# Kernel tuning notes

Measured on AMD Instinct MI355X. Metric: run time of the kernel, lower is better.

Reference implementation:

```python
import math
import jax, jax.numpy as jnp
from jax import lax
import numpy as np

B, DIM, H, W = 8, 256, 64, 64
D_STATE, D_CONV, EXPAND = 16, 4, 2
D_INNER = EXPAND * DIM
DT_RANK = math.ceil(DIM / 16)
POS_LEN = 16
EPS = 1e-5
GN_GROUPS = 32


def setup_inputs() -> dict:
    key = jax.random.key(0)
    ks = iter(jax.random.split(key, 24))
    rn = lambda shape, s=0.02: jax.random.normal(next(ks), shape, jnp.float32) * s
    inp = {}
    inp["x"] = jax.random.normal(next(ks), (B, DIM, H, W), jnp.float32)
    inp["pos_emb"] = rn((1, DIM, POS_LEN), 1.0)
    inp["ln_g"] = jnp.ones((DIM,), jnp.float32)
    inp["ln_b"] = jnp.zeros((DIM,), jnp.float32)
    inp["m_in_w"] = rn((2, 2 * D_INNER, DIM))
    inp["m_conv_w"] = rn((2, D_INNER, D_CONV), 0.1)
    inp["m_conv_b"] = jnp.zeros((2, D_INNER), jnp.float32)
    inp["m_xproj_w"] = rn((2, DT_RANK + 2 * D_STATE, D_INNER))
    inp["m_dt_w"] = rn((2, D_INNER, DT_RANK), 0.1)
    inp["m_dt_b"] = rn((2, D_INNER), 0.1)
    inp["m_A_log"] = jnp.tile(jnp.log(jnp.arange(1, D_STATE + 1, dtype=jnp.float32))[None, None, :], (2, D_INNER, 1))
    inp["m_D"] = jnp.ones((2, D_INNER), jnp.float32)
    inp["m_out_w"] = rn((2, DIM, D_INNER))
    inp["proj_w"] = rn((DIM, 2 * DIM))
    inp["proj_b"] = jnp.zeros((DIM,), jnp.float32)
    inp["up_dw_w"] = rn((DIM, 1, 3, 3), 0.1)
    inp["up_bn1_g"] = jnp.ones((DIM,), jnp.float32)
    inp["up_bn1_b"] = jnp.zeros((DIM,), jnp.float32)
    inp["up_pw_w"] = rn((DIM, DIM), 0.05)
    inp["up_bn2_g"] = jnp.ones((DIM,), jnp.float32)
    inp["up_bn2_b"] = jnp.zeros((DIM,), jnp.float32)
    inp["down_pw_w"] = rn((DIM, DIM), 0.05)
    inp["down_bn_g"] = jnp.ones((DIM,), jnp.float32)
    inp["down_bn_b"] = jnp.zeros((DIM,), jnp.float32)
    inp["gn_g"] = jnp.ones((DIM,), jnp.float32)
    inp["gn_b"] = jnp.zeros((DIM,), jnp.float32)
    return inp


def reference(x, pos_emb, ln_g, ln_b, m_in_w, m_conv_w, m_conv_b, m_xproj_w, m_dt_w, m_dt_b,
              m_A_log, m_D, m_out_w, proj_w, proj_b, up_dw_w, up_bn1_g, up_bn1_b, up_pw_w,
              up_bn2_g, up_bn2_b, down_pw_w, down_bn_g, down_bn_b, gn_g, gn_b):
    Bx, C, Hh, Ww = x.shape

    def ln(t):  # LayerNorm over last dim (shared self.norm)
        m = jnp.mean(t, -1, keepdims=True)
        v = jnp.mean((t - m) ** 2, -1, keepdims=True)
        return (t - m) * lax.rsqrt(v + EPS) * ln_g + ln_b

    def bn(t, g, b):  # BatchNorm2d in eval mode with default running stats (mean 0, var 1)
        return t * (g / jnp.sqrt(1.0 + EPS))[None, :, None, None] + b[None, :, None, None]

    def gn(t):  # GroupNorm(32, C), shared params (self.bn)
        Bn, Cn, Hn, Wn = t.shape
        tg = t.reshape(Bn, GN_GROUPS, Cn // GN_GROUPS, Hn, Wn)
        m = jnp.mean(tg, (2, 3, 4), keepdims=True)
        v = jnp.mean((tg - m) ** 2, (2, 3, 4), keepdims=True)
        tg = (tg - m) * lax.rsqrt(v + EPS)
        return tg.reshape(Bn, Cn, Hn, Wn) * gn_g[None, :, None, None] + gn_b[None, :, None, None]

    def interp_pos(N):  # F.interpolate(pos_embed, size=N, mode='linear', align_corners=False)
        coords = jnp.maximum((jnp.arange(N, dtype=jnp.float32) + 0.5) * (POS_LEN / N) - 0.5, 0.0)
        i0 = jnp.floor(coords).astype(jnp.int32)
        i1 = jnp.minimum(i0 + 1, POS_LEN - 1)
        wgt = coords - i0.astype(jnp.float32)
        return pos_emb[:, :, i0] * (1.0 - wgt) + pos_emb[:, :, i1] * wgt  # (1,C,N)

    def pe_branch(vals, idx, N):  # vals (B,C,N); indices interp at same size = identity
        t = vals + interp_pos(N) + idx.astype(jnp.float32)
        return ln(jnp.swapaxes(t, 1, 2))  # (B,N,C)

    def mamba(u, d):  # standard mamba_ssm selective scan; u (B,L,C)
        xz = jnp.einsum('blc,ic->bli', u, m_in_w[d])
        xh, zg = jnp.split(xz, 2, -1)
        xc = lax.conv_general_dilated(jnp.swapaxes(xh, 1, 2), m_conv_w[d][:, None, :], (1,),
                                      [(D_CONV - 1, 0)], feature_group_count=D_INNER,
                                      dimension_numbers=('NCH', 'OIH', 'NCH'))
        xc = jnp.swapaxes(jax.nn.silu(xc + m_conv_b[d][None, :, None]), 1, 2)  # (B,L,di)
        dbl = jnp.einsum('bld,ed->ble', xc, m_xproj_w[d])
        dt = dbl[..., :DT_RANK]
        Bm = dbl[..., DT_RANK:DT_RANK + D_STATE]
        Cm = dbl[..., DT_RANK + D_STATE:]
        dt = jax.nn.softplus(jnp.einsum('blr,dr->bld', dt, m_dt_w[d]) + m_dt_b[d])  # (B,L,di)
        A = -jnp.exp(m_A_log[d])  # (di,ds)
        dA = jnp.exp(dt[..., None] * A)  # (B,L,di,ds)
        dBx = dt[..., None] * Bm[:, :, None, :] * xc[..., None]

        def step(h, inps):
            dA_t, dBx_t, C_t = inps
            h = dA_t * h + dBx_t
            return h, jnp.einsum('bds,bs->bd', h, C_t)

        h0 = jnp.zeros((u.shape[0], D_INNER, D_STATE), u.dtype)
        _, ys = lax.scan(step, h0, (jnp.swapaxes(dA, 0, 1), jnp.swapaxes(dBx, 0, 1), jnp.swapaxes(Cm, 0, 1)))
        y = jnp.swapaxes(ys, 0, 1) + xc * m_D[d]
        y = y * jax.nn.silu(zg)
        return jnp.einsum('bld,od->blo', y, m_out_w[d])

    # z branch: depthwise ConvTranspose2d(k3,s2,p1,op1) + BN + ReLU + pw conv + BN, then ReLU6
    z = lax.conv_general_dilated(x, jnp.flip(up_dw_w, (2, 3)), (1, 1), [(1, 2), (1, 2)],
                                 lhs_dilation=(2, 2), feature_group_count=C,
                                 dimension_numbers=('NCHW', 'OIHW', 'NCHW'))  # (B,C,2H,2W)
    z = jax.nn.relu(bn(z, up_bn1_g, up_bn1_b))
    z = jnp.einsum('bchw,oc->bohw', z, up_pw_w)
    z = jnp.clip(bn(z, up_bn2_g, up_bn2_b), 0.0, 6.0)

    col_max = pe_branch(jnp.max(x, 2), jnp.argmax(x, 2), Ww)
    col_min = pe_branch(jnp.min(x, 2), jnp.argmin(x, 2), Ww)
    row_max = pe_branch(jnp.max(x, 3), jnp.argmax(x, 3), Hh)
    row_min = pe_branch(jnp.min(x, 3), jnp.argmin(x, 3), Hh)
    result_max = jnp.concatenate([col_max, row_max], 1)  # (B, W+H, C)
    result_min = jnp.concatenate([col_min, row_min], 1)

    fm_max = ln(mamba(result_max, 0))
    fm_min = ln(mamba(result_min, 0))
    bm_max = ln(mamba(jnp.flip(result_max, 1), 1))
    bm_min = ln(mamba(jnp.flip(result_min, 1), 1))

    res_max = jnp.concatenate([fm_max, jnp.flip(bm_max, 1)], -1) @ proj_w.T + proj_b
    res_min = jnp.concatenate([fm_min, jnp.flip(bm_min, 1)], -1) @ proj_w.T + proj_b
    res_max = ln(res_max)[:, :, None, :]  # (B,L,1,C)
    res_min = ln(res_min)[:, None, :, :]  # (B,1,L,C)

    res = jnp.transpose(res_max + res_min, (0, 3, 1, 2))  # (B,C,L,L), L=H+W=2H
    res = jnp.clip(res + 3.0, 0.0, 6.0) / 6.0 * z  # h_sigmoid gate
    res = gn(res)
    res = jnp.einsum('bchw,oc->bohw', res[:, :, ::2, ::2], down_pw_w)  # pw conv stride 2
    res = bn(res, down_bn_g, down_bn_b)
    res = gn(res)
    res = res + x
    res = gn(res)
    return res
```

## Files before the change

kernel.cpp:

```cpp
#include <hip/hip_runtime.h>
#include <hip/hip_bf16.h>
#include <math.h>

typedef __hip_bfloat16 bf16;
typedef __attribute__((ext_vector_type(8))) short short8_t;
typedef __attribute__((ext_vector_type(4))) short short4_t;
typedef __attribute__((ext_vector_type(4))) float f32x4_t;

#define EPSV 1e-5f
#define BNSC 0.99999500003749968f

__device__ __forceinline__ float bf2f(bf16 v){ return __bfloat162float(v); }
__device__ __forceinline__ bf16 f2bf(float v){ return __float2bfloat16(v); }

__device__ __forceinline__ float blk_sum(float v, float* sm){
  int tid = threadIdx.x;
  #pragma unroll
  for(int o=32;o>0;o>>=1) v += __shfl_down(v, o, 64);
  if((tid&63)==0) sm[tid>>6] = v;
  __syncthreads();
  float s = 0.f;
  int nw = blockDim.x>>6;
  for(int i=0;i<nw;i++) s += sm[i];
  __syncthreads();
  return s;
}

__device__ __forceinline__ float softplusf(float x){
  return (x > 20.f) ? x : __logf(1.f + __expf(x));
}
__device__ __forceinline__ float siluf(float x){
  return x / (1.f + __expf(-x));
}

__global__ void prep_weights(const float* __restrict__ in_w, const float* __restrict__ out_w,
                             const float* __restrict__ pw_w, const float* __restrict__ dpw_w,
                             const float* __restrict__ proj_w,
                             bf16* __restrict__ Winb, bf16* __restrict__ Woutb,
                             bf16* __restrict__ Wub, bf16* __restrict__ Wdb,
                             float* __restrict__ PT, float* __restrict__ gacc){
  int idx = blockIdx.x*256 + threadIdx.x;
  if(idx < 6656) gacc[idx] = 0.f;
  if(idx < 524288){ Winb[idx] = f2bf(in_w[idx]); return; }
  if(idx < 786432){ int i=idx-524288; Woutb[i] = f2bf(out_w[i]); return; }
  if(idx < 851968){ int i=idx-786432; Wub[i] = f2bf(pw_w[i]); return; }
  if(idx < 917504){ int i=idx-851968; Wdb[i] = f2bf(dpw_w[i]); return; }
  int k = idx - 917504;
  int i = k >> 9, j = k & 511;
  PT[j*256 + i] = proj_w[k];
}

__global__ __launch_bounds__(256)
void r1_reduce_pe(const float* __restrict__ x, const float* __restrict__ pe,
                  float* __restrict__ pmax, float* __restrict__ pmin,
                  float* __restrict__ xs, float* __restrict__ xq){
  __shared__ float tile[64*65];
  __shared__ float rs_[4], rq_[4];
  int bc = blockIdx.x;
  int b = bc >> 8, c = bc & 255;
  const float* xp = x + ((size_t)bc << 12);
  float s = 0.f, q = 0.f;
  for(int i=threadIdx.x; i<4096; i+=256){
    float v = xp[i];
    tile[(i>>6)*65 + (i&63)] = v;
    s += v; q += v*v;
  }
  #pragma unroll
  for(int o=32;o>0;o>>=1){ s += __shfl_down(s, o, 64); q += __shfl_down(q, o, 64); }
  int wv = threadIdx.x >> 6, t = threadIdx.x & 63;
  if(t == 0){ rs_[wv] = s; rq_[wv] = q; }
  __syncthreads();
  if(threadIdx.x == 0){
    xs[bc] = rs_[0]+rs_[1]+rs_[2]+rs_[3];
    xq[bc] = rq_[0]+rq_[1]+rq_[2]+rq_[3];
  }
  if(wv >= 2) return;
  float coords = fmaxf((t + 0.5f)*0.25f - 0.5f, 0.f);
  int i0 = (int)floorf(coords);
  int i1 = min(i0+1, 15);
  float wg = coords - (float)i0;
  float pos = pe[c*16+i0]*(1.f-wg) + pe[c*16+i1]*wg;
  if(wv == 0){
    float cmx=-3.4e38f, cmn=3.4e38f; int cax=0, can=0;
    for(int h=0;h<64;h++){
      float v = tile[h*65 + t];
      if(v > cmx){ cmx=v; cax=h; }
      if(v < cmn){ cmn=v; can=h; }
    }
    size_t base_col = ((size_t)b*128 + t)*256 + c;
    pmax[base_col] = cmx + pos + (float)cax;
    pmin[base_col] = cmn + pos + (float)can;
  } else {
    float rmx=-3.4e38f, rmn=3.4e38f; int rax=0, ran=0;
    for(int w=0;w<64;w++){
      float v = tile[t*65 + w];
      if(v > rmx){ rmx=v; rax=w; }
      if(v < rmn){ rmn=v; ran=w; }
    }
    size_t base_row = ((size_t)b*128 + 64 + t)*256 + c;
    pmax[base_row] = rmx + pos + (float)rax;
    pmin[base_row] = rmn + pos + (float)ran;
  }
}

__global__ void ln_rows2(float* __restrict__ bufA, float* __restrict__ bufB,
                         const float* __restrict__ g, const float* __restrict__ bb,
                         bf16* __restrict__ boutA, bf16* __restrict__ boutB){
  __shared__ float sm[8];
  int row = blockIdx.x, t = threadIdx.x;
  float* buf; bf16* bout;
  if(row < 1024){ buf = bufA; bout = boutA; }
  else { buf = bufB; bout = boutB; row -= 1024; }
  float v = buf[(size_t)row*256 + t];
  float m = blk_sum(v, sm) * (1.f/256.f);
  float dv = v - m;
  float var = blk_sum(dv*dv, sm) * (1.f/256.f);
  float r = dv * rsqrtf(var + EPSV) * g[t] + bb[t];
  buf[(size_t)row*256 + t] = r;
  if(bout) bout[(size_t)row*256 + t] = f2bf(r);
}

__global__ __launch_bounds__(256,2)
void m1_mfma(const bf16* __restrict__ ubmax, const bf16* __restrict__ ubmin,
             const bf16* __restrict__ Win, float* __restrict__ xz){
  __shared__ bf16 att[64*264];
  int bx = blockIdx.x;
  int it = bx & 3, lt = (bx>>2)&1, b = (bx>>3)&7, r = bx>>6;
  int d = r & 1;
  const bf16* u = (r < 2) ? ubmax : ubmin;
  int flip = r & 1;
  int t = threadIdx.x;
  {
    int pr = t>>5, cc = (t&31)*8;
    #pragma unroll
    for(int i=0;i<8;i++){
      int p = pr + i*8;
      int l = lt*64 + p;
      int le = flip ? (127 - l) : l;
      short8_t v = *(const short8_t*)((const short*)u + ((size_t)(b*128 + le))*256 + cc);
      *(short8_t*)&att[p*264 + cc] = v;
    }
  }
  __syncthreads();
  int wv = t>>6, lane = t&63, quad = lane>>4, l16 = lane&15;
  int m0 = wv*64;
  f32x4_t acc[4][4];
  #pragma unroll
  for(int ms=0;ms<4;ms++)
    #pragma unroll
    for(int ns=0;ns<4;ns++) acc[ms][ns] = (f32x4_t){0.f,0.f,0.f,0.f};
  const short* wbase = (const short*)Win + ((size_t)d*1024 + it*256)*256;
  for(int k0=0;k0<256;k0+=32){
    short8_t afr[4], bfr[4];
    #pragma unroll
    for(int ms=0;ms<4;ms++)
      afr[ms] = *(const short8_t*)(wbase + (size_t)(m0 + ms*16 + l16)*256 + k0 + quad*8);
    #pragma unroll
    for(int ns=0;ns<4;ns++)
      bfr[ns] = *(const short8_t*)&att[(ns*16 + l16)*264 + k0 + quad*8];
    #pragma unroll
    for(int ms=0;ms<4;ms++)
      #pragma unroll
      for(int ns=0;ns<4;ns++)
        acc[ms][ns] = __builtin_amdgcn_mfma_f32_16x16x32_bf16(afr[ms], bfr[ns], acc[ms][ns], 0,0,0);
  }
  int rb = r*8 + b;
  #pragma unroll
  for(int ns=0;ns<4;ns++){
    int l = lt*64 + ns*16 + l16;
    float* dst = xz + ((size_t)rb*128 + l)*1024 + it*256;
    #pragma unroll
    for(int ms=0;ms<4;ms++){
      int i = m0 + ms*16 + quad*4;
      *(f32x4_t*)(dst + i) = acc[ms][ns];
    }
  }
}

#define LSEG4 4
__global__ __launch_bounds__(256)
void m234(const float* __restrict__ xz, const float* __restrict__ cw,
          const float* __restrict__ cb, const float* __restrict__ xproj,
          const float* __restrict__ dtw, const float* __restrict__ dtbias,
          float* __restrict__ xc, float* __restrict__ dbl, float* __restrict__ dt){
  __shared__ float xcs[LSEG4*512];
  __shared__ float pbuf[LSEG4*48*4];
  __shared__ float dblrow[LSEG4*48];
  int bx = blockIdx.x;
  int rb = bx >> 5, seg = bx & 31;
  int l0 = seg * LSEG4;
  int d = (rb >> 3) & 1;
  int t = threadIdx.x;
  #pragma unroll
  for(int j=0; j<(LSEG4*512)/256; j++){
    int i = t + j*256;
    int lr = i >> 9, dd = i & 511;
    int gl = l0 + lr;
    const float* src = xz + ((size_t)rb*128 + gl)*1024 + dd;
    f32x4_t wv = *(const f32x4_t*)(cw + (size_t)(d*512 + dd)*4);
    float s = cb[d*512 + dd];
    float v0 = (gl >= 3) ? src[-3*1024] : 0.f;
    float v1 = (gl >= 2) ? src[-2*1024] : 0.f;
    float v2 = (gl >= 1) ? src[-1*1024] : 0.f;
    float v3 = src[0];
    s += v0*wv[0] + v1*wv[1] + v2*wv[2] + v3*wv[3];
    s = siluf(s);
    xcs[i] = s;
    xc[((size_t)(rb*128 + gl))*512 + dd] = s;
  }
  __syncthreads();
  #pragma unroll
  for(int j=0; j<3; j++){
    int id = t + j*256;
    int row = id / 192;
    int rem = id - row*192;
    int e = rem >> 2, part = rem & 3;
    const float* wp = xproj + ((size_t)(d*48 + e)*512) + part*128;
    const float* xr = xcs + row*512 + part*128;
    float s = 0.f;
    #pragma unroll 4
    for(int k4=0; k4<32; k4++){
      f32x4_t wv = *(const f32x4_t*)(wp + k4*4);
      f32x4_t xv = *(const f32x4_t*)(xr + k4*4);
      s += wv[0]*xv[0] + wv[1]*xv[1] + wv[2]*xv[2] + wv[3]*xv[3];
    }
    pbuf[id] = s;
  }
  __syncthreads();
  for(int i=t; i<LSEG4*48; i+=256){
    int row = i / 48, e = i - row*48;
    int base = row*192 + e*4;
    float s = pbuf[base] + pbuf[base+1] + pbuf[base+2] + pbuf[base+3];
    dblrow[i] = s;
    dbl[((size_t)(rb*128 + l0 + row))*48 + e] = s;
  }
  __syncthreads();
  #pragma unroll
  for(int j=0; j<(LSEG4*512)/256; j++){
    int i = t + j*256;
    int row = i >> 9, dd = i & 511;
    const float* wp = dtw + (size_t)(d*512 + dd)*16;
    const float* dr = dblrow + row*48;
    float s = dtbias[d*512 + dd];
    #pragma unroll
    for(int r4=0; r4<4; r4++){
      f32x4_t wv = *(const f32x4_t*)(wp + r4*4);
      s += dr[r4*4+0]*wv[0] + dr[r4*4+1]*wv[1] + dr[r4*4+2]*wv[2] + dr[r4*4+3]*wv[3];
    }
    dt[((size_t)(rb*128 + l0 + row))*512 + dd] = softplusf(s);
  }
}

__global__ void m5_passA(const float* __restrict__ dt, const float* __restrict__ xc,
                         const float* __restrict__ dbl, const float* __restrict__ Alog,
                         float* __restrict__ P, float* __restrict__ Hl){
  int bx = blockIdx.x;
  int seg = bx & 7, half = (bx>>3)&1, rb = bx>>4;
  int dd = half*256 + threadIdx.x;
  int d = (rb>>3)&1;
  float A[16], h[16], pr[16];
  #pragma unroll
  for(int s=0;s<16;s++){
    A[s] = -__expf(Alog[(size_t)(d*512 + dd)*16 + s]);
    h[s] = 0.f; pr[s] = 1.f;
  }
  int l0 = seg*16;
  for(int l=l0;l<l0+16;l++){
    size_t row = (size_t)rb*128 + l;
    float dtv = dt[row*512 + dd];
    float xcv = xc[row*512 + dd];
    float bx_ = dtv*xcv;
    const float* dr = dbl + row*48;
    #pragma unroll
    for(int s=0;s<16;s++){
      float dA = __expf(dtv*A[s]);
      pr[s] *= dA;
      h[s] = dA*h[s] + bx_*dr[16+s];
    }
  }
  size_t o = ((size_t)(rb*8 + seg)*512 + dd)*16;
  #pragma unroll
  for(int s=0;s<16;s+=4){
    *(f32x4_t*)(P  + o + s) = (f32x4_t){pr[s],pr[s+1],pr[s+2],pr[s+3]};
    *(f32x4_t*)(Hl + o + s) = (f32x4_t){h[s],h[s+1],h[s+2],h[s+3]};
  }
}

__global__ void m5_passB(const float* __restrict__ dt, const float* __restrict__ xc,
                         const float* __restrict__ dbl, const float* __restrict__ xz,
                         const float* __restrict__ Alog, const float* __restrict__ Dp,
                         const float* __restrict__ P, const float* __restrict__ Hl,
                         bf16* __restrict__ ybb){
  int bx = blockIdx.x;
  int seg = bx & 7, half = (bx>>3)&1, rb = bx>>4;
  int dd = half*256 + threadIdx.x;
  int d = (rb>>3)&1;
  float A[16], h[16];
  #pragma unroll
  for(int s=0;s<16;s++){
    A[s] = -__expf(Alog[(size_t)(d*512 + dd)*16 + s]);
    h[s] = 0.f;
  }
  for(int j=0;j<seg;j++){
    size_t o = ((size_t)(rb*8 + j)*512 + dd)*16;
    #pragma unroll
    for(int s=0;s<16;s+=4){
      f32x4_t pv = *(const f32x4_t*)(P + o + s);
      f32x4_t hv = *(const f32x4_t*)(Hl + o + s);
      h[s]   = pv[0]*h[s]   + hv[0];
      h[s+1] = pv[1]*h[s+1] + hv[1];
      h[s+2] = pv[2]*h[s+2] + hv[2];
      h[s+3] = pv[3]*h[s+3] + hv[3];
    }
  }
  float Dv = Dp[d*512 + dd];
  int l0 = seg*16;
  for(int l=l0;l<l0+16;l++){
    size_t row = (size_t)rb*128 + l;
    float dtv = dt[row*512 + dd];
    float xcv = xc[row*512 + dd];
    float zgv = xz[row*1024 + 512 + dd];
    const float* dr = dbl + row*48;
    float bx_ = dtv*xcv;
    float y = 0.f;
    #pragma unroll
    for(int s=0;s<16;s++){
      h[s] = __expf(dtv*A[s])*h[s] + bx_*dr[16+s];
      y += h[s]*dr[32+s];
    }
    ybb[row*512 + dd] = f2bf((y + xcv*Dv) * siluf(zgv));
  }
}

__global__ __launch_bounds__(256,2)
void m6_mfma(const bf16* __restrict__ ybb, const bf16* __restrict__ Wout,
             const float* __restrict__ lng, const float* __restrict__ lnb,
             float* __restrict__ mo){
  __shared__ char smem[64*264*4];
  bf16* ybt = (bf16*)smem;
  float* fbuf = (float*)smem;
  int bx = blockIdx.x;
  int lt = bx & 1, b = (bx>>1)&7, r = bx>>4;
  int d = r & 1, rb = r*8 + b;
  size_t rowbase = (size_t)rb*128 + lt*64;
  int t = threadIdx.x;
  for(int i=t;i<4096;i+=256){
    int row = i>>6, c8 = (i&63)*8;
    short8_t v = *(const short8_t*)((const short*)ybb + (rowbase + row)*512 + c8);
    *(short8_t*)&ybt[row*520 + c8] = v;
  }
  __syncthreads();
  int wv = t>>6, lane = t&63, quad = lane>>4, l16 = lane&15;
  int m0 = wv*64;
  f32x4_t acc[4][4];
  #pragma unroll
  for(int ms=0;ms<4;ms++)
    #pragma unroll
    for(int ns=0;ns<4;ns++) acc[ms][ns] = (f32x4_t){0.f,0.f,0.f,0.f};
  const short* wbase = (const short*)Wout + (size_t)d*256*512;
  for(int k0=0;k0<512;k0+=32){
    short8_t afr[4], bfr[4];
    #pragma unroll
    for(int ms=0;ms<4;ms++)
      afr[ms] = *(const short8_t*)(wbase + (size_t)(m0 + ms*16 + l16)*512 + k0 + quad*8);
    #pragma unroll
    for(int ns=0;ns<4;ns++)
      bfr[ns] = *(const short8_t*)&ybt[(ns*16 + l16)*520 + k0 + quad*8];
    #pragma unroll
    for(int ms=0;ms<4;ms++)
      #pragma unroll
      for(int ns=0;ns<4;ns++)
        acc[ms][ns] = __builtin_amdgcn_mfma_f32_16x16x32_bf16(afr[ms], bfr[ns], acc[ms][ns], 0,0,0);
  }
  __syncthreads();
  #pragma unroll
  for(int ns=0;ns<4;ns++){
    int row = ns*16 + l16;
    #pragma unroll
    for(int ms=0;ms<4;ms++){
      int o = m0 + ms*16 + quad*4;
      *(f32x4_t*)(fbuf + row*264 + o) = acc[ms][ns];
    }
  }
  __syncthreads();
  {
    int row = t >> 2, part = t & 3;
    const float* fr = fbuf + row*264;
    float s = 0.f;
    #pragma unroll 8
    for(int j=0;j<64;j++){
      int col = part*64 + ((j + part*16) & 63);
      s += fr[col];
    }
    s += __shfl_xor(s, 1, 64);
    s += __shfl_xor(s, 2, 64);
    float m = s * (1.f/256.f);
    float q = 0.f;
    #pragma unroll 8
    for(int j=0;j<64;j++){
      int col = part*64 + ((j + part*16) & 63);
      float dv = fr[col] - m;
      q += dv*dv;
    }
    q += __shfl_xor(q, 1, 64);
    q += __shfl_xor(q, 2, 64);
    float rs = rsqrtf(q*(1.f/256.f) + EPSV);
    float* dst = mo + (rowbase + row)*256;
    for(int j=0;j<64;j++){
      int col = part*64 + j;
      dst[col] = (fr[col] - m)*rs*lng[col] + lnb[col];
    }
  }
}

__global__ void m7_proj(const float* __restrict__ mo, const float* __restrict__ PT,
                        const float* __restrict__ pb, const float* __restrict__ lng,
                        const float* __restrict__ lnb, float* __restrict__ resm,
                        float* __restrict__ resn){
  __shared__ float ct[16*512];
  __shared__ float fbuf[16*264];
  int bx = blockIdx.x;
  int tt = bx >> 6, rem = bx & 63, b = rem >> 3, lt = rem & 7;
  int fr_ = tt*2, br = tt*2 + 1;
  for(int i=threadIdx.x;i<16*512;i+=256){
    int lr = i >> 9, k = i & 511;
    int l = lt*16 + lr;
    ct[i] = (k < 256)
      ? mo[(((size_t)(fr_*8+b)*128) + l)*256 + k]
      : mo[(((size_t)(br*8+b)*128) + (127-l))*256 + (k-256)];
  }
  __syncthreads();
  float acc[16];
  #pragma unroll
  for(int q=0;q<16;q++) acc[q] = 0.f;
  int t = threadIdx.x;
  for(int k=0;k<512;k++){
    float pv = PT[(size_t)k*256 + t];
    #pragma unroll
    for(int q=0;q<16;q++) acc[q] += pv * ct[(q<<9) + k];
  }
  float bias = pb[t];
  #pragma unroll
  for(int q=0;q<16;q++) fbuf[q*264 + t] = acc[q] + bias;
  __syncthreads();
  float* dstbuf = tt ? resn : resm;
  if(t < 64){
    int row = t >> 2, part = t & 3;
    const float* fr = fbuf + row*264;
    float s = 0.f;
    for(int j=0;j<64;j++){
      int col = part*64 + ((j + part*16) & 63);
      s += fr[col];
    }
    s += __shfl_xor(s, 1, 64);
    s += __shfl_xor(s, 2, 64);
    float m = s * (1.f/256.f);
    float q = 0.f;
    for(int j=0;j<64;j++){
      int col = part*64 + ((j + part*16) & 63);
      float dv = fr[col] - m;
      q += dv*dv;
    }
    q += __shfl_xor(q, 1, 64);
    q += __shfl_xor(q, 2, 64);
    float rs = rsqrtf(q*(1.f/256.f) + EPSV);
    float* dst = dstbuf + ((size_t)b*128 + lt*16 + row)*256;
    for(int j=0;j<64;j++){
      int col = part*64 + j;
      dst[col] = (fr[col] - m)*rs*lng[col] + lnb[col];
    }
  }
}

__global__ __launch_bounds__(256)
void k1_deconv_T(const float* __restrict__ x, const float* __restrict__ wdw,
                 const float* __restrict__ g1, const float* __restrict__ b1,
                 bf16* __restrict__ zT){
  __shared__ float in[2*64*33];
  __shared__ bf16 ot[64*80];
  int bx = blockIdx.x;
  int cb = bx & 3, half = (bx>>2)&1, h = (bx>>3)&127, b = bx>>10;
  int c0 = cb*64, w0 = half*64, iw0 = w0>>1;
  int h_odd = h & 1;
  int ihA = h_odd ? (h-1)>>1 : h>>1;
  int ihB = (h+1)>>1;
  bool hasB = h_odd && (ihB < 64);
  for(int i = threadIdx.x; i < 4224; i += 256){
    int row = i / 2112;
    int rem = i - row*2112;
    int c = rem / 33;
    int iw = rem - c*33;
    int ihl = row ? ihB : ihA;
    bool valid = (iw0 + iw < 64) && (row == 0 || hasB);
    in[i] = valid ? x[(((size_t)b*256 + c0 + c)<<12) + (ihl<<6) + iw0 + iw] : 0.f;
  }
  __syncthreads();
  int c = threadIdx.x & 63, g = threadIdx.x >> 6;
  const float* wp = wdw + (c0+c)*9;
  int khA3 = h_odd ? 6 : 3;
  float wA0 = wp[khA3], wA1 = wp[khA3+1], wA2 = wp[khA3+2];
  float wB0 = wp[0],    wB1 = wp[1],      wB2 = wp[2];
  float scale = g1[c0+c]*BNSC, bias = b1[c0+c];
  const float* inA = in + c*33;
  const float* inB = in + 2112 + c*33;
  #pragma unroll
  for(int i=0;i<16;i++){
    int wi = g*16 + i;
    float s;
    if(!(i&1)){
      int iw = wi>>1;
      s = inA[iw]*wA1 + inB[iw]*wB1;
    } else {
      int iwa = (wi-1)>>1, iwb = (wi+1)>>1;
      s = inA[iwa]*wA2 + inA[iwb]*wA0 + inB[iwa]*wB2 + inB[iwb]*wB0;
    }
    ot[wi*80 + c] = f2bf(fmaxf(s*scale + bias, 0.f));
  }
  __syncthreads();
  int rr = threadIdx.x >> 3;
  int co = (threadIdx.x & 7) * 8;
  size_t obase = (((size_t)b*16384) + (size_t)h*128 + w0)*256 + c0;
  #pragma unroll
  for(int pass=0; pass<2; pass++){
    int wi = rr + pass*32;
    short8_t v = *(const short8_t*)&ot[wi*80 + co];
    *(short8_t*)((short*)zT + obase + (size_t)wi*256 + co) = v;
  }
}

__global__ __launch_bounds__(256,2)
void k2_mfma(const bf16* __restrict__ zT, const bf16* __restrict__ Wub,
             const float* __restrict__ g2, const float* __restrict__ b2,
             const float* __restrict__ resm, const float* __restrict__ resn,
             bf16* __restrict__ resS, float* __restrict__ gsum1, float* __restrict__ gssq1){
  __shared__ bf16 zt[128*264];
  __shared__ float rm_s[256];
  __shared__ float gn_s[32], gn_q[32];
  int b = blockIdx.y;
  int p0 = blockIdx.x*128;
  int h = p0 >> 7;
  int t = threadIdx.x;
  if(t < 32){ gn_s[t] = 0.f; gn_q[t] = 0.f; }
  if(t >= 64 && t < 128){
    int tt = t - 64;
    *(f32x4_t*)&rm_s[tt*4] = *(const f32x4_t*)(resm + ((size_t)b*128 + h)*256 + tt*4);
  }
  {
    const short* src = (const short*)zT + (((size_t)b*16384 + p0)*256);
    int pr = t>>5;
    int cc = (t&31)*8;
    #pragma unroll
    for(int i=0;i<16;i++){
      int p = pr + i*8;
      short8_t v = *(const short8_t*)(src + (size_t)p*256 + cc);
      *(short8_t*)&zt[p*264 + cc] = v;
    }
  }
  __syncthreads();
  int wv = t>>6, lane = t&63, quad = lane>>4, l16 = lane&15;
  int m0 = wv*64;
  f32x4_t acc[4][8];
  #pragma unroll
  for(int ms=0;ms<4;ms++)
    #pragma unroll
    for(int ns=0;ns<8;ns++) acc[ms][ns] = (f32x4_t){0.f,0.f,0.f,0.f};
  const short* wp = (const short*)Wub + (size_t)(m0 + l16)*256 + quad*8;
  short8_t afr[4];
  #pragma unroll
  for(int ms=0;ms<4;ms++) afr[ms] = *(const short8_t*)(wp + (size_t)ms*16*256);
  for(int k0=0;k0<256;k0+=32){
    short8_t anext[4];
    if(k0 + 32 < 256){
      #pragma unroll
      for(int ms=0;ms<4;ms++)
        anext[ms] = *(const short8_t*)(wp + (size_t)ms*16*256 + k0 + 32);
    }
    short8_t bfr[8];
    #pragma unroll
    for(int ns=0;ns<8;ns++)
      bfr[ns] = *(const short8_t*)&zt[(ns*16 + l16)*264 + k0 + quad*8];
    #pragma unroll
    for(int ms=0;ms<4;ms++)
      #pragma unroll
      for(int ns=0;ns<8;ns++)
        acc[ms][ns] = __builtin_amdgcn_mfma_f32_16x16x32_bf16(afr[ms], bfr[ns], acc[ms][ns], 0,0,0);
    #pragma unroll
    for(int ms=0;ms<4;ms++) afr[ms] = anext[ms];
  }
  __syncthreads();
  bool h_even = ((h & 1) == 0);
  float sg[4], qg[4];
  #pragma unroll
  for(int ms=0;ms<4;ms++){ sg[ms]=0.f; qg[ms]=0.f; }
  #pragma unroll
  for(int ns=0;ns<8;ns++){
    int pl = ns*16 + l16;
    const float* rn = resn + ((size_t)b*128 + pl)*256;
    bool store = h_even && ((pl & 1) == 0);
    #pragma unroll
    for(int ms=0;ms<4;ms++){
      int o = m0 + ms*16 + quad*4;
      f32x4_t a = acc[ms][ns];
      f32x4_t gv = *(const f32x4_t*)(g2+o);
      f32x4_t bv = *(const f32x4_t*)(b2+o);
      f32x4_t rmv = *(const f32x4_t*)&rm_s[o];
      f32x4_t rnv = *(const f32x4_t*)(rn+o);
      alignas(8) bf16 ov[4];
      #pragma unroll
      for(int r=0;r<4;r++){
        float zv = a[r]*(gv[r]*BNSC) + bv[r];
        zv = fminf(fmaxf(zv, 0.f), 6.f);
        float gate = fminf(fmaxf(rmv[r]+rnv[r]+3.f, 0.f), 6.f)*(1.f/6.f);
        float vo = zv*gate;
        ov[r] = f2bf(vo);
        sg[ms] += vo;
        qg[ms] += vo*vo;
      }
      if(store) *(short4_t*)&zt[pl*264 + o] = *(const short4_t*)ov;
    }
  }
  #pragma unroll
  for(int ms=0;ms<4;ms++){
    float S = sg[ms], Q = qg[ms];
    S += __shfl_xor(S, 1, 64);  Q += __shfl_xor(Q, 1, 64);
    S += __shfl_xor(S, 2, 64);  Q += __shfl_xor(Q, 2, 64);
    S += __shfl_xor(S, 4, 64);  Q += __shfl_xor(Q, 4, 64);
    S += __shfl_xor(S, 8, 64);  Q += __shfl_xor(Q, 8, 64);
    if(l16 == 0){
      int o = m0 + ms*16 + quad*4;
      atomicAdd(&gn_s[o>>3], S);
      atomicAdd(&gn_q[o>>3], Q);
    }
  }
  __syncthreads();
  if(t < 32){
    atomicAdd(&gsum1[b*32 + t], gn_s[t]);
    atomicAdd(&gssq1[b*32 + t], gn_q[t]);
  }
  if(h_even){
    short* dst = (short*)resS + ((size_t)b*4096 + (h>>1)*64)*256;
    #pragma unroll
    for(int it=0; it<8; it++){
      int slot = t + it*256;
      int row = slot >> 5;
      int co = (slot & 31)*8;
      short8_t v = *(const short8_t*)&zt[(row*2)*264 + co];
      *(short8_t*)(dst + (size_t)row*256 + co) = v;
    }
  }
}

__global__ __launch_bounds__(256,2)
void k4_mfma(const bf16* __restrict__ resS, const bf16* __restrict__ Wdb,
             const float* __restrict__ gsum1, const float* __restrict__ gssq1,
             const float* __restrict__ gng, const float* __restrict__ gnb,
             const float* __restrict__ dbg, const float* __restrict__ dbb,
             const float* __restrict__ x, float* __restrict__ t1,
             float* __restrict__ t1s, float* __restrict__ t1q, float* __restrict__ t1x){
  __shared__ bf16 at[128*264];
  __shared__ float sc[256], sb[256];
  __shared__ float stm[32], str[32];
  int b = blockIdx.y;
  int q0 = blockIdx.x*128;
  int t = threadIdx.x;
  if(t < 32){
    float m = gsum1[b*32+t] * (1.f/131072.f);
    float var = gssq1[b*32+t] * (1.f/131072.f) - m*m;
    stm[t] = m;
    str[t] = rsqrtf(var + EPSV);
  }
  __syncthreads();
  {
    int cch = t, g = cch>>3;
    float m = stm[g], rs = str[g];
    float s = rs*gng[cch];
    sc[cch] = s; sb[cch] = gnb[cch] - m*s;
  }
  __syncthreads();
  {
    int pr = t>>5;
    int cc = (t&31)*8;
    const short* src = (const short*)resS + ((size_t)b*4096 + q0)*256;
    #pragma unroll
    for(int i=0;i<16;i++){
      int q = pr + i*8;
      short8_t v = *(const short8_t*)(src + (size_t)q*256 + cc);
      const bf16* vv = (const bf16*)&v;
      alignas(16) bf16 ov[8];
      #pragma unroll
      for(int j=0;j<8;j++) ov[j] = f2bf(bf2f(vv[j])*sc[cc+j] + sb[cc+j]);
      *(short8_t*)&at[q*264 + cc] = *(const short8_t*)ov;
    }
  }
  __syncthreads();
  int wv = t>>6, lane = t&63, quad = lane>>4, l16 = lane&15;
  int n0 = wv*64;
  f32x4_t acc[8][4];
  #pragma unroll
  for(int ms=0;ms<8;ms++)
    #pragma unroll
    for(int ns=0;ns<4;ns++) acc[ms][ns] = (f32x4_t){0.f,0.f,0.f,0.f};
  const short* wp = (const short*)Wdb + (size_t)(n0 + l16)*256 + quad*8;
  short8_t bfr[4];
  #pragma unroll
  for(int ns=0;ns<4;ns++) bfr[ns] = *(const short8_t*)(wp + (size_t)ns*16*256);
  for(int k0=0;k0<256;k0+=32){
    short8_t bnext[4];
    if(k0 + 32 < 256){
      #pragma unroll
      for(int ns=0;ns<4;ns++)
        bnext[ns] = *(const short8_t*)(wp + (size_t)ns*16*256 + k0 + 32);
    }
    short8_t afr[8];
    #pragma unroll
    for(int ms=0;ms<8;ms++)
      afr[ms] = *(const short8_t*)&at[(ms*16 + l16)*264 + k0 + quad*8];
    #pragma unroll
    for(int ms=0;ms<8;ms++)
      #pragma unroll
      for(int ns=0;ns<4;ns++)
        acc[ms][ns] = __builtin_amdgcn_mfma_f32_16x16x32_bf16(afr[ms], bfr[ns], acc[ms][ns], 0,0,0);
    #pragma unroll
    for(int ns=0;ns<4;ns++) bfr[ns] = bnext[ns];
  }
  #pragma unroll
  for(int ns=0;ns<4;ns++){
    int o = n0 + ns*16 + l16;
    float s2 = dbg[o]*BNSC, bb2 = dbb[o];
    float* dst = t1 + (((size_t)b*256 + o) << 12);
    const float* xsrc = x + (((size_t)b*256 + o) << 12);
    float s_=0.f, q_=0.f, c_=0.f;
    #pragma unroll
    for(int ms=0;ms<8;ms++){
      int ps = q0 + ms*16 + quad*4;
      f32x4_t a = acc[ms][ns];
      f32x4_t xv = *(const f32x4_t*)(xsrc + ps);
      f32x4_t ov;
      #pragma unroll
      for(int r=0;r<4;r++){
        ov[r] = a[r]*s2 + bb2;
        s_ += ov[r];
        q_ += ov[r]*ov[r];
        c_ += ov[r]*xv[r];
      }
      *(f32x4_t*)(dst + ps) = ov;
    }
    s_ += __shfl_xor(s_, 16, 64);
    q_ += __shfl_xor(q_, 16, 64);
    c_ += __shfl_xor(c_, 16, 64);
    s_ += __shfl_xor(s_, 32, 64);
    q_ += __shfl_xor(q_, 32, 64);
    c_ += __shfl_xor(c_, 32, 64);
    if(quad == 0){
      atomicAdd(&t1s[b*256 + o], s_);
      atomicAdd(&t1q[b*256 + o], q_);
      atomicAdd(&t1x[b*256 + o], c_);
    }
  }
}

__global__ void compose_gn(const float* __restrict__ t1s, const float* __restrict__ t1q,
                           const float* __restrict__ t1x, const float* __restrict__ xs,
                           const float* __restrict__ xq, const float* __restrict__ gng,
                           const float* __restrict__ gnb,
                           float* __restrict__ cA, float* __restrict__ cB, float* __restrict__ cC){
  int b = blockIdx.x, c = threadIdx.x;
  int i = b*256 + c;
  float ts = t1s[i], tq = t1q[i], tx = t1x[i];
  float sx = xs[i], qx = xq[i];
  float gs = ts, gq = tq;
  gs += __shfl_xor(gs,1,64); gq += __shfl_xor(gq,1,64);
  gs += __shfl_xor(gs,2,64); gq += __shfl_xor(gq,2,64);
  gs += __shfl_xor(gs,4,64); gq += __shfl_xor(gq,4,64);
  float m2 = gs*(1.f/32768.f);
  float v2 = gq*(1.f/32768.f) - m2*m2;
  float rs2 = rsqrtf(v2 + EPSV);
  float a  = rs2*gng[c];
  float bb = gnb[c] - m2*a;
  float Su = a*ts + 4096.f*bb + sx;
  float Qu = a*a*tq + 4096.f*bb*bb + qx + 2.f*a*bb*ts + 2.f*a*tx + 2.f*bb*sx;
  float gSu = Su, gQu = Qu;
  gSu += __shfl_xor(gSu,1,64); gQu += __shfl_xor(gQu,1,64);
  gSu += __shfl_xor(gSu,2,64); gQu += __shfl_xor(gQu,2,64);
  gSu += __shfl_xor(gSu,4,64); gQu += __shfl_xor(gQu,4,64);
  float m3 = gSu*(1.f/32768.f);
  float v3 = gQu*(1.f/32768.f) - m3*m3;
  float rs3 = rsqrtf(v3 + EPSV);
  float s3 = rs3*gng[c];
  cA[i] = a*s3;
  cB[i] = s3;
  cC[i] = (bb - m3)*s3 + gnb[c];
}

__global__ void k8_gn_out(const float* __restrict__ t1, const float* __restrict__ x,
                          const float* __restrict__ cA, const float* __restrict__ cB,
                          const float* __restrict__ cC, float* __restrict__ out){
  int i4 = blockIdx.x*256 + threadIdx.x;
  int idx = i4 << 2;
  int c = (idx >> 12) & 255, b = idx >> 20;
  int i = b*256 + c;
  float A = cA[i], Bv = cB[i], C = cC[i];
  f32x4_t tv = *(const f32x4_t*)(t1 + idx);
  f32x4_t xv = *(const f32x4_t*)(x + idx);
  f32x4_t ov;
  #pragma unroll
  for(int r=0;r<4;r++) ov[r] = A*tv[r] + Bv*xv[r] + C;
  *(f32x4_t*)(out + idx) = ov;
}

extern "C" void kernel_launch(void* const* d_in, const int* in_sizes, int n_in,
                              void* d_out, int out_size, void* d_ws, size_t ws_size,
                              hipStream_t stream){
  const float* x      = (const float*)d_in[0];
  const float* pos    = (const float*)d_in[1];
  const float* ln_g   = (const float*)d_in[2];
  const float* ln_b   = (const float*)d_in[3];
  const float* in_w   = (const float*)d_in[4];
  const float* conv_w = (const float*)d_in[5];
  const float* conv_b = (const float*)d_in[6];
  const float* xproj  = (const float*)d_in[7];
  const float* dt_w   = (const float*)d_in[8];
  const float* dt_b   = (const float*)d_in[9];
  const float* A_log  = (const float*)d_in[10];
  const float* Dp     = (const float*)d_in[11];
  const float* out_w  = (const float*)d_in[12];
  const float* proj_w = (const float*)d_in[13];
  const float* proj_b = (const float*)d_in[14];
  const float* dw_w   = (const float*)d_in[15];
  const float* bn1g   = (const float*)d_in[16];
  const float* bn1b   = (const float*)d_in[17];
  const float* pw_w   = (const float*)d_in[18];
  const float* bn2g   = (const float*)d_in[19];
  const float* bn2b   = (const float*)d_in[20];
  const float* dpw_w  = (const float*)d_in[21];
  const float* dbng   = (const float*)d_in[22];
  const float* dbnb   = (const float*)d_in[23];
  const float* gng    = (const float*)d_in[24];
  const float* gnb    = (const float*)d_in[25];
  float* out = (float*)d_out;

  float* ws = (float*)d_ws;
  bf16*  resS = (bf16*)ws;
  bf16*  zT   = (bf16*)(ws + 16777216);
  float* scanP = ws + 16777216;
  float* scanH = ws + 16777216 + 2097152;
  float* zone = ws + 33554432;
  float* xz   = zone;
  float* xc   = xz  + 4194304;
  float* dbl  = xc  + 2097152;
  float* dtb  = dbl + 196608;
  bf16*  ybb  = (bf16*)(dtb + 2097152);
  float* t1   = zone;
  float* mo   = zone + 9633792;
  float* resm = mo   + 1048576;
  float* resn = resm + 262144;
  float* pmax = resn + 262144;
  float* pmin = pmax + 262144;
  float* PT   = pmin + 262144;
  bf16*  ubmax= (bf16*)(PT + 131072);
  bf16*  ubmin= (bf16*)(PT + 131072 + 131072);
  bf16*  Winb = (bf16*)(PT + 131072 + 262144);
  bf16*  Woutb= (bf16*)(PT + 131072 + 524288);
  bf16*  Wub  = (bf16*)(PT + 131072 + 655360);
  bf16*  Wdb  = (bf16*)(PT + 131072 + 688128);
  float* gacc = PT + 131072 + 720896;
  float* gsum1 = gacc,        *gssq1 = gacc + 256;
  float* t1s = gacc + 512;
  float* t1q = gacc + 2560;
  float* t1x = gacc + 4608;
  float* xs  = gacc + 6656;
  float* xq  = gacc + 8704;
  float* cA  = gacc + 10752;
  float* cB  = gacc + 12800;
  float* cC  = gacc + 14848;

  prep_weights<<<4096,256,0,stream>>>(in_w, out_w, pw_w, dpw_w, proj_w,
                                      Winb, Woutb, Wub, Wdb, PT, gacc);

  r1_reduce_pe<<<2048,256,0,stream>>>(x, pos, pmax, pmin, xs, xq);
  ln_rows2<<<2048,256,0,stream>>>(pmax, pmin, ln_g, ln_b, ubmax, ubmin);

  m1_mfma<<<256,256,0,stream>>>(ubmax, ubmin, Winb, xz);
  m234<<<1024,256,0,stream>>>(xz, conv_w, conv_b, xproj, dt_w, dt_b, xc, dbl, dtb);
  m5_passA<<<512,256,0,stream>>>(dtb, xc, dbl, A_log, scanP, scanH);
  m5_passB<<<512,256,0,stream>>>(dtb, xc, dbl, xz, A_log, Dp, scanP, scanH, ybb);
  m6_mfma<<<64,256,0,stream>>>(ybb, Woutb, ln_g, ln_b, mo);
  m7_proj<<<128,256,0,stream>>>(mo, PT, proj_b, ln_g, ln_b, resm, resn);

  k1_deconv_T<<<8192,256,0,stream>>>(x, dw_w, bn1g, bn1b, zT);
  k2_mfma<<<dim3(128,8),256,0,stream>>>(zT, Wub, bn2g, bn2b, resm, resn, resS,
                                        gsum1, gssq1);

  k4_mfma<<<dim3(32,8),256,0,stream>>>(resS, Wdb, gsum1, gssq1,
                                       gng, gnb, dbng, dbnb, x, t1, t1s, t1q, t1x);

  compose_gn<<<8,256,0,stream>>>(t1s, t1q, t1x, xs, xq, gng, gnb, cA, cB, cC);
  k8_gn_out<<<8192,256,0,stream>>>(t1, x, cA, cB, cC, out);
}
```

Measured before the change: 485.1 us.

## Split fused conv/xproj/dt kernel into three kernels with MFMA x_proj

New measurement: 464.4 us. -4.3%, faster.

```diff
diff --git a/kernel.cpp b/kernel.cpp
--- a/kernel.cpp
+++ b/kernel.cpp
@@ -35,19 +35,25 @@
 
 __global__ void prep_weights(const float* __restrict__ in_w, const float* __restrict__ out_w,
                              const float* __restrict__ pw_w, const float* __restrict__ dpw_w,
-                             const float* __restrict__ proj_w,
+                             const float* __restrict__ proj_w, const float* __restrict__ xproj_w,
                              bf16* __restrict__ Winb, bf16* __restrict__ Woutb,
                              bf16* __restrict__ Wub, bf16* __restrict__ Wdb,
-                             float* __restrict__ PT, float* __restrict__ gacc){
+                             bf16* __restrict__ Wxpb, float* __restrict__ PT,
+                             float* __restrict__ gacc){
   int idx = blockIdx.x*256 + threadIdx.x;
   if(idx < 6656) gacc[idx] = 0.f;
   if(idx < 524288){ Winb[idx] = f2bf(in_w[idx]); return; }
   if(idx < 786432){ int i=idx-524288; Woutb[i] = f2bf(out_w[i]); return; }
   if(idx < 851968){ int i=idx-786432; Wub[i] = f2bf(pw_w[i]); return; }
   if(idx < 917504){ int i=idx-851968; Wdb[i] = f2bf(dpw_w[i]); return; }
-  int k = idx - 917504;
-  int i = k >> 9, j = k & 511;
-  PT[j*256 + i] = proj_w[k];
+  if(idx < 1048576){
+    int k = idx - 917504;
+    int i = k >> 9, j = k & 511;
+    PT[j*256 + i] = proj_w[k];
+    return;
+  }
+  int i = idx - 1048576;
+  Wxpb[i] = f2bf(xproj_w[i]);
 }
 
 __global__ __launch_bounds__(256)
@@ -177,78 +183,98 @@
   }
 }
 
-#define LSEG4 4
 __global__ __launch_bounds__(256)
-void m234(const float* __restrict__ xz, const float* __restrict__ cw,
-          const float* __restrict__ cb, const float* __restrict__ xproj,
-          const float* __restrict__ dtw, const float* __restrict__ dtbias,
-          float* __restrict__ xc, float* __restrict__ dbl, float* __restrict__ dt){
-  __shared__ float xcs[LSEG4*512];
-  __shared__ float pbuf[LSEG4*48*4];
-  __shared__ float dblrow[LSEG4*48];
-  int bx = blockIdx.x;
-  int rb = bx >> 5, seg = bx & 31;
-  int l0 = seg * LSEG4;
-  int d = (rb >> 3) & 1;
+void m2_conv(const float* __restrict__ xz, const float* __restrict__ cw,
+             const float* __restrict__ cb, float* __restrict__ xc,
+             bf16* __restrict__ xcb){
+  int i4 = blockIdx.x*256 + threadIdx.x;
+  int idx = i4 << 2;
+  int row = idx >> 9, dd = idx & 511;
+  int gl = row & 127;
+  int d = (row >> 10) & 1;
+  const float* src = xz + (size_t)row*1024 + dd;
+  const float* cwp = cw + (size_t)(d*512 + dd)*4;
+  f32x4_t w0 = *(const f32x4_t*)(cwp);
+  f32x4_t w1 = *(const f32x4_t*)(cwp+4);
+  f32x4_t w2 = *(const f32x4_t*)(cwp+8);
+  f32x4_t w3 = *(const f32x4_t*)(cwp+12);
+  f32x4_t bias = *(const f32x4_t*)(cb + d*512 + dd);
+  f32x4_t z4 = (f32x4_t){0.f,0.f,0.f,0.f};
+  f32x4_t t3 = *(const f32x4_t*)(src);
+  f32x4_t t2 = (gl>=1) ? *(const f32x4_t*)(src-1024) : z4;
+  f32x4_t t1 = (gl>=2) ? *(const f32x4_t*)(src-2048) : z4;
+  f32x4_t t0 = (gl>=3) ? *(const f32x4_t*)(src-3072) : z4;
+  f32x4_t o;
+  o[0] = bias[0] + t0[0]*w0[0] + t1[0]*w0[1] + t2[0]*w0[2] + t3[0]*w0[3];
+  o[1] = bias[1] + t0[1]*w1[0] + t1[1]*w1[1] + t2[1]*w1[2] + t3[1]*w1[3];
+  o[2] = bias[2] + t0[2]*w2[0] + t1[2]*w2[1] + t2[2]*w2[2] + t3[2]*w2[3];
+  o[3] = bias[3] + t0[3]*w3[0] + t1[3]*w3[1] + t2[3]*w3[2] + t3[3]*w3[3];
+  alignas(8) bf16 ob[4];
+  #pragma unroll
+  for(int r=0;r<4;r++){ o[r] = siluf(o[r]); ob[r] = f2bf(o[r]); }
+  *(f32x4_t*)(xc + idx) = o;
+  *(short4_t*)((short*)xcb + idx) = *(const short4_t*)ob;
+}
+
+__global__ __launch_bounds__(256)
+void m3_xproj(const bf16* __restrict__ xcb, const bf16* __restrict__ Wxpb,
+              float* __restrict__ dbl){
+  int r0 = blockIdx.x * 64;
+  int d = (r0 >> 10) & 1;
   int t = threadIdx.x;
-  #pragma unroll
-  for(int j=0; j<(LSEG4*512)/256; j++){
-    int i = t + j*256;
-    int lr = i >> 9, dd = i & 511;
-    int gl = l0 + lr;
-    const float* src = xz + ((size_t)rb*128 + gl)*1024 + dd;
-    f32x4_t wv = *(const f32x4_t*)(cw + (size_t)(d*512 + dd)*4);
-    float s = cb[d*512 + dd];
-    float v0 = (gl >= 3) ? src[-3*1024] : 0.f;
-    float v1 = (gl >= 2) ? src[-2*1024] : 0.f;
-    float v2 = (gl >= 1) ? src[-1*1024] : 0.f;
-    float v3 = src[0];
-    s += v0*wv[0] + v1*wv[1] + v2*wv[2] + v3*wv[3];
-    s = siluf(s);
-    xcs[i] = s;
-    xc[((size_t)(rb*128 + gl))*512 + dd] = s;
-  }
-  __syncthreads();
-  #pragma unroll
-  for(int j=0; j<3; j++){
-    int id = t + j*256;
-    int row = id / 192;
-    int rem = id - row*192;
-    int e = rem >> 2, part = rem & 3;
-    const float* wp = xproj + ((size_t)(d*48 + e)*512) + part*128;
-    const float* xr = xcs + row*512 + part*128;
-    float s = 0.f;
-    #pragma unroll 4
-    for(int k4=0; k4<32; k4++){
-      f32x4_t wv = *(const f32x4_t*)(wp + k4*4);
-      f32x4_t xv = *(const f32x4_t*)(xr + k4*4);
-      s += wv[0]*xv[0] + wv[1]*xv[1] + wv[2]*xv[2] + wv[3]*xv[3];
-    }
-    pbuf[id] = s;
-  }
-  __syncthreads();
-  for(int i=t; i<LSEG4*48; i+=256){
-    int row = i / 48, e = i - row*48;
-    int base = row*192 + e*4;
-    float s = pbuf[base] + pbuf[base+1] + pbuf[base+2] + pbuf[base+3];
-    dblrow[i] = s;
-    dbl[((size_t)(rb*128 + l0 + row))*48 + e] = s;
-  }
-  __syncthreads();
-  #pragma unroll
-  for(int j=0; j<(LSEG4*512)/256; j++){
-    int i = t + j*256;
-    int row = i >> 9, dd = i & 511;
-    const float* wp = dtw + (size_t)(d*512 + dd)*16;
-    const float* dr = dblrow + row*48;
-    float s = dtbias[d*512 + dd];
-    #pragma unroll
-    for(int r4=0; r4<4; r4++){
-      f32x4_t wv = *(const f32x4_t*)(wp + r4*4);
-      s += dr[r4*4+0]*wv[0] + dr[r4*4+1]*wv[1] + dr[r4*4+2]*wv[2] + dr[r4*4+3]*wv[3];
-    }
-    dt[((size_t)(rb*128 + l0 + row))*512 + dd] = softplusf(s);
-  }
+  int wv = t>>6, lane = t&63, quad = lane>>4, l16 = lane&15;
+  int rowl = wv*16 + l16;
+  const short* bbase = (const short*)xcb + (size_t)(r0 + rowl)*512;
+  const short* abase = (const short*)Wxpb + (size_t)d*48*512;
+  f32x4_t acc[3];
+  #pragma unroll
+  for(int ms=0;ms<3;ms++) acc[ms] = (f32x4_t){0.f,0.f,0.f,0.f};
+  #pragma unroll 4
+  for(int k0=0;k0<512;k0+=32){
+    short8_t bfr = *(const short8_t*)(bbase + k0 + quad*8);
+    short8_t afr[3];
+    #pragma unroll
+    for(int ms=0;ms<3;ms++)
+      afr[ms] = *(const short8_t*)(abase + (size_t)(ms*16 + l16)*512 + k0 + quad*8);
+    #pragma unroll
+    for(int ms=0;ms<3;ms++)
+      acc[ms] = __builtin_amdgcn_mfma_f32_16x16x32_bf16(afr[ms], bfr, acc[ms], 0,0,0);
+  }
+  float* dst = dbl + (size_t)(r0 + rowl)*48;
+  #pragma unroll
+  for(int ms=0;ms<3;ms++)
+    *(f32x4_t*)(dst + ms*16 + quad*4) = acc[ms];
+}
+
+__global__ __launch_bounds__(256)
+void m4_dt(const float* __restrict__ dbl, const float* __restrict__ dtw,
+           const float* __restrict__ dtbias, float* __restrict__ dt){
+  int i4 = blockIdx.x*256 + threadIdx.x;
+  int idx = i4 << 2;
+  int row = idx >> 9, dd = idx & 511;
+  int d = (row >> 10) & 1;
+  const float* dr = dbl + (size_t)row*48;
+  f32x4_t dr0 = *(const f32x4_t*)(dr);
+  f32x4_t dr1 = *(const f32x4_t*)(dr+4);
+  f32x4_t dr2 = *(const f32x4_t*)(dr+8);
+  f32x4_t dr3 = *(const f32x4_t*)(dr+12);
+  f32x4_t bias = *(const f32x4_t*)(dtbias + d*512 + dd);
+  f32x4_t o;
+  #pragma unroll
+  for(int j=0;j<4;j++){
+    const float* wp = dtw + (size_t)(d*512 + dd + j)*16;
+    f32x4_t w0 = *(const f32x4_t*)(wp);
+    f32x4_t w1 = *(const f32x4_t*)(wp+4);
+    f32x4_t w2 = *(const f32x4_t*)(wp+8);
+    f32x4_t w3 = *(const f32x4_t*)(wp+12);
+    float s = bias[j];
+    s += dr0[0]*w0[0] + dr0[1]*w0[1] + dr0[2]*w0[2] + dr0[3]*w0[3];
+    s += dr1[0]*w1[0] + dr1[1]*w1[1] + dr1[2]*w1[2] + dr1[3]*w1[3];
+    s += dr2[0]*w2[0] + dr2[1]*w2[1] + dr2[2]*w2[2] + dr2[3]*w2[3];
+    s += dr3[0]*w3[0] + dr3[1]*w3[1] + dr3[2]*w3[2] + dr3[3]*w3[3];
+    o[j] = softplusf(s);
+  }
+  *(f32x4_t*)(dt + idx) = o;
 }
 
 __global__ void m5_passA(const float* __restrict__ dt, const float* __restrict__ xc,
@@ -850,6 +876,7 @@
   float* dbl  = xc  + 2097152;
   float* dtb  = dbl + 196608;
   bf16*  ybb  = (bf16*)(dtb + 2097152);
+  bf16*  xcb  = (bf16*)(dtb + 2097152 + 524288);
   float* t1   = zone;
   float* mo   = zone + 9633792;
   float* resm = mo   + 1048576;
@@ -863,7 +890,8 @@
   bf16*  Woutb= (bf16*)(PT + 131072 + 524288);
   bf16*  Wub  = (bf16*)(PT + 131072 + 655360);
   bf16*  Wdb  = (bf16*)(PT + 131072 + 688128);
-  float* gacc = PT + 131072 + 720896;
+  bf16*  Wxpb = (bf16*)(PT + 131072 + 720896);
+  float* gacc = PT + 131072 + 745472;
   float* gsum1 = gacc,        *gssq1 = gacc + 256;
   float* t1s = gacc + 512;
   float* t1q = gacc + 2560;
@@ -874,14 +902,16 @@
   float* cB  = gacc + 12800;
   float* cC  = gacc + 14848;
 
-  prep_weights<<<4096,256,0,stream>>>(in_w, out_w, pw_w, dpw_w, proj_w,
-                                      Winb, Woutb, Wub, Wdb, PT, gacc);
+  prep_weights<<<4288,256,0,stream>>>(in_w, out_w, pw_w, dpw_w, proj_w, xproj,
+                                      Winb, Woutb, Wub, Wdb, Wxpb, PT, gacc);
 
   r1_reduce_pe<<<2048,256,0,stream>>>(x, pos, pmax, pmin, xs, xq);
   ln_rows2<<<2048,256,0,stream>>>(pmax, pmin, ln_g, ln_b, ubmax, ubmin);
 
   m1_mfma<<<256,256,0,stream>>>(ubmax, ubmin, Winb, xz);
-  m234<<<1024,256,0,stream>>>(xz, conv_w, conv_b, xproj, dt_w, dt_b, xc, dbl, dtb);
+  m2_conv<<<2048,256,0,stream>>>(xz, conv_w, conv_b, xc, xcb);
+  m3_xproj<<<64,256,0,stream>>>(xcb, Wxpb, dbl);
+  m4_dt<<<2048,256,0,stream>>>(dbl, dt_w, dt_b, dtb);
   m5_passA<<<512,256,0,stream>>>(dtb, xc, dbl, A_log, scanP, scanH);
   m5_passB<<<512,256,0,stream>>>(dtb, xc, dbl, xz, A_log, Dp, scanP, scanH, ybb);
   m6_mfma<<<64,256,0,stream>>>(ybb, Woutb, ln_g, ln_b, mo);
```
